# Kernel tuning notes

Measured on AMD Instinct MI355X. Metric: run time of the kernel, lower is better.

The kernel has to match this reference:

```python
import jax, jax.numpy as jnp
import numpy as np

B, T, C = 2, 2048, 1024
H, DH = 16, 64            # n_head, head_size; H*DH == C
HID = 4096                # FFN hidden
EPS = 1e-5


def setup_inputs() -> dict:
    key = jax.random.key(0)
    ks = jax.random.split(key, 16)
    s_c = 1.0 / np.sqrt(C)
    s_h = 1.0 / np.sqrt(HID)
    return {
        "x": jax.random.normal(ks[0], (B, T, C), jnp.float32),
        "ln1_g": jnp.ones((C,), jnp.float32),
        "ln1_b": jnp.zeros((C,), jnp.float32),
        "Wq": jax.random.normal(ks[1], (H, C, DH), jnp.float32) * s_c,
        "Wk": jax.random.normal(ks[2], (H, C, DH), jnp.float32) * s_c,
        "Wv": jax.random.normal(ks[3], (H, C, DH), jnp.float32) * s_c,
        "Wo": jax.random.normal(ks[4], (C, C), jnp.float32) * s_c,
        "bo": jnp.zeros((C,), jnp.float32),
        "ln2_g": jnp.ones((C,), jnp.float32),
        "ln2_b": jnp.zeros((C,), jnp.float32),
        "W1": jax.random.normal(ks[5], (C, HID), jnp.float32) * s_c,
        "b1": jnp.zeros((HID,), jnp.float32),
        "W2": jax.random.normal(ks[6], (HID, C), jnp.float32) * s_h,
        "b2": jnp.zeros((C,), jnp.float32),
    }


def _layernorm(x, g, b):
    mu = jnp.mean(x, axis=-1, keepdims=True)
    var = jnp.mean(jnp.square(x - mu), axis=-1, keepdims=True)
    return (x - mu) * jax.lax.rsqrt(var + EPS) * g + b


def _block(x, ln1_g, ln1_b, Wq, Wk, Wv, Wo, bo, ln2_g, ln2_b, W1, b1, W2, b2):
    # --- self-attention (note: scale by C**-0.5, as in original code) ---
    h = _layernorm(x, ln1_g, ln1_b)                      # [B,T,C]
    q = jnp.einsum("btc,hcd->bhtd", h, Wq)
    k = jnp.einsum("btc,hcd->bhtd", h, Wk)
    v = jnp.einsum("btc,hcd->bhtd", h, Wv)
    wei = jnp.einsum("bhtd,bhsd->bhts", q, k) * (C ** -0.5)
    causal = jnp.tril(jnp.ones((T, T), bool))            # [T,T]
    wei = jnp.where(causal, wei, -jnp.inf)
    wei = jax.nn.softmax(wei, axis=-1)
    att = jnp.einsum("bhts,bhsd->bhtd", wei, v)          # [B,H,T,DH]
    att = att.transpose(0, 2, 1, 3).reshape(x.shape[0], x.shape[1], C)  # concat heads
    x = x + att @ Wo + bo
    # --- feed-forward ---
    h2 = _layernorm(x, ln2_g, ln2_b)
    x = x + jax.nn.relu(h2 @ W1 + b1) @ W2 + b2
    return x


def reference(x, ln1_g, ln1_b, Wq, Wk, Wv, Wo, bo, ln2_g, ln2_b, W1, b1, W2, b2):
    return _block(x, ln1_g, ln1_b, Wq, Wk, Wv, Wo, bo, ln2_g, ln2_b, W1, b1, W2, b2)
```

## Files before the change

### kernel.cpp

```cpp
#include <hip/hip_runtime.h>

typedef unsigned short ushort_t;
typedef __attribute__((ext_vector_type(8))) short short8;
typedef __attribute__((ext_vector_type(4))) float f32x4;

#define BT 4096
#define TSEQ 2048
#define CC 1024
#define NH 16
#define DH 64
#define HID 4096
#define ATT_SCALE 0.03125f

__device__ __forceinline__ ushort_t f2bf(float f) {
    unsigned u = __float_as_uint(f);
    u = u + 0x7fffu + ((u >> 16) & 1u);
    return (ushort_t)(u >> 16);
}

typedef const __attribute__((address_space(1))) unsigned int* gptr_t;
typedef __attribute__((address_space(3))) unsigned int* lptr_t;
__device__ __forceinline__ void gload_lds16(const void* g, void* l) {
    __builtin_amdgcn_global_load_lds((gptr_t)g, (lptr_t)l, 16, 0, 0);
}

__global__ __launch_bounds__(256) void transpose_cvt(
    const float* __restrict__ in, ushort_t* __restrict__ out, int R, int Cn)
{
    __shared__ float tile[32][33];
    size_t off = (size_t)blockIdx.z * R * Cn;
    int c0 = blockIdx.x * 32, r0 = blockIdx.y * 32;
    int tx = threadIdx.x & 31, ty = threadIdx.x >> 5;
#pragma unroll
    for (int q = 0; q < 4; ++q)
        tile[ty + 8 * q][tx] = in[off + (size_t)(r0 + ty + 8 * q) * Cn + c0 + tx];
    __syncthreads();
#pragma unroll
    for (int q = 0; q < 4; ++q)
        out[off + (size_t)(c0 + ty + 8 * q) * R + r0 + tx] = f2bf(tile[tx][ty + 8 * q]);
}

__global__ __launch_bounds__(256) void ln_kernel(
    const float* __restrict__ x, const float* __restrict__ g,
    const float* __restrict__ b, ushort_t* __restrict__ out)
{
    int row = blockIdx.x;
    const float4 xv = ((const float4*)(x + (size_t)row * CC))[threadIdx.x];
    float s = xv.x + xv.y + xv.z + xv.w;
    float s2 = xv.x * xv.x + xv.y * xv.y + xv.z * xv.z + xv.w * xv.w;
#pragma unroll
    for (int d = 1; d < 64; d <<= 1) {
        s += __shfl_xor(s, d);
        s2 += __shfl_xor(s2, d);
    }
    __shared__ float ps[4], ps2[4];
    int w = threadIdx.x >> 6, lane = threadIdx.x & 63;
    if (lane == 0) { ps[w] = s; ps2[w] = s2; }
    __syncthreads();
    s = ps[0] + ps[1] + ps[2] + ps[3];
    s2 = ps2[0] + ps2[1] + ps2[2] + ps2[3];
    float mu = s * (1.0f / CC);
    float var = s2 * (1.0f / CC) - mu * mu;
    float rs = rsqrtf(var + 1e-5f);
    int c = threadIdx.x * 4;
    const float4 gv = ((const float4*)g)[threadIdx.x];
    const float4 bv = ((const float4*)b)[threadIdx.x];
    ushort_t u0 = f2bf((xv.x - mu) * rs * gv.x + bv.x);
    ushort_t u1 = f2bf((xv.y - mu) * rs * gv.y + bv.y);
    ushort_t u2 = f2bf((xv.z - mu) * rs * gv.z + bv.z);
    ushort_t u3 = f2bf((xv.w - mu) * rs * gv.w + bv.w);
    unsigned lo = (unsigned)u0 | ((unsigned)u1 << 16);
    unsigned hi = (unsigned)u2 | ((unsigned)u3 << 16);
    ((uint2*)(out + (size_t)row * CC + c))[0] = make_uint2(lo, hi);
}

template <int BM, int BN, int WM, int WN, int MR, int NR, int MODE>
__global__ __launch_bounds__(256) void gemm_tile(
    const ushort_t* __restrict__ A, const ushort_t* __restrict__ Bt,
    int N, int K,
    const float* __restrict__ bias, const float* __restrict__ resid,
    void* __restrict__ out0, void* __restrict__ out1, void* __restrict__ out2)
{
    static_assert(WM * WN == 4 && WM * MR * 16 == BM && WN * NR * 16 == BN, "geom");
    __shared__ ushort_t As[BM * 32];
    __shared__ ushort_t Bs[BN * 32];

    const int t = threadIdx.x;
    const int w = t >> 6, lane = t & 63, g = lane >> 4, c = lane & 15;
    const int wr = w / WN, wc = w % WN;
    const int m0 = blockIdx.x * BM;
    const int n0 = blockIdx.y * BN;

    f32x4 acc[MR][NR];
#pragma unroll
    for (int mi = 0; mi < MR; ++mi)
#pragma unroll
        for (int ni = 0; ni < NR; ++ni) acc[mi][ni] = f32x4{0.f, 0.f, 0.f, 0.f};

    const ushort_t* Ard = As + (size_t)(wr * MR * 16 + c) * 32 + g * 8;
    const ushort_t* Brd = Bs + (size_t)(wc * NR * 16 + c) * 32 + g * 8;
    const int arow = t >> 2, acol = (t & 3) * 8;

    for (int k0 = 0; k0 < K; k0 += 32) {
        __syncthreads();
#pragma unroll
        for (int j = 0; j < BM / 64; ++j)
            gload_lds16(A + (size_t)(m0 + j * 64 + arow) * K + k0 + acol,
                        As + (size_t)j * 2048 + t * 8);
#pragma unroll
        for (int j = 0; j < BN / 64; ++j)
            gload_lds16(Bt + (size_t)(n0 + j * 64 + arow) * K + k0 + acol,
                        Bs + (size_t)j * 2048 + t * 8);
        __syncthreads();

        short8 af[MR], bf[NR];
#pragma unroll
        for (int mi = 0; mi < MR; ++mi) af[mi] = *(const short8*)(Ard + mi * 512);
#pragma unroll
        for (int ni = 0; ni < NR; ++ni) bf[ni] = *(const short8*)(Brd + ni * 512);
#pragma unroll
        for (int mi = 0; mi < MR; ++mi)
#pragma unroll
            for (int ni = 0; ni < NR; ++ni)
                acc[mi][ni] = __builtin_amdgcn_mfma_f32_16x16x32_bf16(
                    af[mi], bf[ni], acc[mi][ni], 0, 0, 0);
    }

#pragma unroll
    for (int mi = 0; mi < MR; ++mi)
#pragma unroll
        for (int ni = 0; ni < NR; ++ni)
#pragma unroll
            for (int i = 0; i < 4; ++i) {
                int row = m0 + wr * MR * 16 + mi * 16 + g * 4 + i;
                int col = n0 + wc * NR * 16 + ni * 16 + c;
                float v = acc[mi][ni][i];
                if (MODE == 0) {
                    v += bias[col] + resid[(size_t)row * N + col];
                    ((float*)out0)[(size_t)row * N + col] = v;
                } else if (MODE == 1) {
                    v += bias[col];
                    v = v > 0.f ? v : 0.f;
                    ((ushort_t*)out0)[(size_t)row * N + col] = f2bf(v);
                } else {
                    int bb = row >> 11, tt = row & (TSEQ - 1);
                    if (col < 1024) {
                        int head = col >> 6, d = col & 63;
                        ((ushort_t*)out0)[((size_t)(bb * NH + head) * TSEQ + tt) * DH + d] =
                            f2bf(v * ATT_SCALE);
                    } else if (col < 2048) {
                        int head = (col - 1024) >> 6, d = col & 63;
                        ((ushort_t*)out1)[((size_t)(bb * NH + head) * TSEQ + tt) * DH + d] = f2bf(v);
                    } else {
                        int head = (col - 2048) >> 6, d = col & 63;
                        ((ushort_t*)out2)[((size_t)(bb * NH + head) * DH + d) * TSEQ + tt] = f2bf(v);
                    }
                }
            }
}

#define FLASH_BODY(st, kc, kn, PREF_COND, MASK_COND)                               \
    {                                                                              \
        const int S0 = (st) * 64;                                                  \
        short8 vv[4][2];                                                           \
        _Pragma("unroll") for (int nf = 0; nf < 4; ++nf)                           \
            _Pragma("unroll") for (int ks = 0; ks < 2; ++ks)                       \
                vv[nf][ks] = *(const short8*)(vp + (size_t)(nf * 16 + c) * TSEQ +  \
                                              S0 + ks * 32 + g * 8);               \
        if (PREF_COND) {                                                           \
            _Pragma("unroll") for (int sub = 0; sub < 4; ++sub)                    \
                _Pragma("unroll") for (int ks = 0; ks < 2; ++ks)                   \
                    kn[sub][ks] = *(const short8*)(kp +                            \
                        (size_t)(S0 + 64 + 16 * sub + c) * DH + ks * 32 + g * 8);  \
        }                                                                          \
        f32x4 sa[4];                                                               \
        _Pragma("unroll") for (int sub = 0; sub < 4; ++sub) {                      \
            f32x4 t0 = f32x4{0.f, 0.f, 0.f, 0.f};                                  \
            t0 = __builtin_amdgcn_mfma_f32_16x16x32_bf16(kc[sub][0], bq0, t0, 0, 0, 0); \
            t0 = __builtin_amdgcn_mfma_f32_16x16x32_bf16(kc[sub][1], bq1, t0, 0, 0, 0); \
            sa[sub] = t0;                                                          \
        }                                                                          \
        float pvv[16];                                                             \
        _Pragma("unroll") for (int sub = 0; sub < 4; ++sub)                        \
            _Pragma("unroll") for (int i = 0; i < 4; ++i) pvv[4 * sub + i] = sa[sub][i]; \
        if (MASK_COND) {                                                           \
            _Pragma("unroll") for (int sub = 0; sub < 4; ++sub)                    \
                _Pragma("unroll") for (int i = 0; i < 4; ++i)                      \
                    if (S0 + 16 * sub + 4 * g + i > q0 + c) pvv[4 * sub + i] = -INFINITY; \
        }                                                                          \
        float tmax = pvv[0];                                                       \
        _Pragma("unroll") for (int j = 1; j < 16; ++j) tmax = fmaxf(tmax, pvv[j]); \
        tmax = fmaxf(tmax, __shfl_xor(tmax, 16));                                  \
        tmax = fmaxf(tmax, __shfl_xor(tmax, 32));                                  \
        if (!__all(tmax - m_ <= 8.0f)) {                                           \
            float mn = fmaxf(m_, tmax);                                            \
            float fac = __expf(m_ - mn);                                           \
            m_ = mn;                                                               \
            l_ *= fac;                                                             \
            _Pragma("unroll") for (int i = 0; i < 4; ++i) {                        \
                float fr = __shfl(fac, 4 * g + i);                                 \
                _Pragma("unroll") for (int nf = 0; nf < 4; ++nf) o[nf][i] *= fr;   \
            }                                                                      \
        }                                                                          \
        float pp[16], rs = 0.f;                                                    \
        _Pragma("unroll") for (int j = 0; j < 16; ++j) {                           \
            pp[j] = __expf(pvv[j] - m_); rs += pp[j];                              \
        }                                                                          \
        rs += __shfl_xor(rs, 16);                                                  \
        rs += __shfl_xor(rs, 32);                                                  \
        l_ += rs;                                                                  \
        _Pragma("unroll") for (int sub = 0; sub < 4; ++sub) {                      \
            unsigned lo = (__float_as_uint(pp[4 * sub + 0]) >> 16) |               \
                          (__float_as_uint(pp[4 * sub + 1]) & 0xffff0000u);        \
            unsigned hi = (__float_as_uint(pp[4 * sub + 2]) >> 16) |               \
                          (__float_as_uint(pp[4 * sub + 3]) & 0xffff0000u);        \
            *(uint2*)(pw + 16 * sub + 4 * g) = make_uint2(lo, hi);                 \
        }                                                                          \
        asm volatile("s_waitcnt lgkmcnt(0)" ::: "memory");                         \
        short8 pa0 = *(const short8*)(&Plds[w][c * 72 + g * 8]);                   \
        short8 pa1 = *(const short8*)(&Plds[w][c * 72 + 32 + g * 8]);              \
        _Pragma("unroll") for (int nf = 0; nf < 4; ++nf) {                         \
            o[nf] = __builtin_amdgcn_mfma_f32_16x16x32_bf16(pa0, vv[nf][0], o[nf], 0, 0, 0); \
            o[nf] = __builtin_amdgcn_mfma_f32_16x16x32_bf16(pa1, vv[nf][1], o[nf], 0, 0, 0); \
        }                                                                          \
    }

__global__ __launch_bounds__(256) void flash_attn(
    const ushort_t* __restrict__ Q, const ushort_t* __restrict__ Kb,
    const ushort_t* __restrict__ Vt, ushort_t* __restrict__ attout)
{
    __shared__ ushort_t Plds[4][16 * 72];
    const int w = threadIdx.x >> 6, lane = threadIdx.x & 63;
    const int g = lane >> 4, c = lane & 15;
    const int bh = blockIdx.x, bb = bh >> 4, hh = bh & 15;
    const int q0 = blockIdx.y * 64 + w * 16;
    const ushort_t* qp = Q + (size_t)bh * TSEQ * DH;
    const ushort_t* kp = Kb + (size_t)bh * TSEQ * DH;
    const ushort_t* vp = Vt + (size_t)bh * DH * TSEQ;

    const short8 bq0 = *(const short8*)(qp + (size_t)(q0 + c) * DH + g * 8);
    const short8 bq1 = *(const short8*)(qp + (size_t)(q0 + c) * DH + 32 + g * 8);

    float m_ = -INFINITY, l_ = 0.f;
    f32x4 o[4];
#pragma unroll
    for (int nf = 0; nf < 4; ++nf) o[nf] = f32x4{0.f, 0.f, 0.f, 0.f};

    const int nst = q0 / 64 + 1;
    ushort_t* pw = &Plds[w][c * 72];

    short8 kkA[4][2], kkB[4][2];
#pragma unroll
    for (int sub = 0; sub < 4; ++sub)
#pragma unroll
        for (int ks = 0; ks < 2; ++ks)
            kkA[sub][ks] = *(const short8*)(kp + (size_t)(16 * sub + c) * DH + ks * 32 + g * 8);

    for (int st = 0; st < nst; st += 2) {
        FLASH_BODY(st, kkA, kkB, (st + 1 < nst), (st == nst - 1));
        if (st + 1 < nst) {
            const int st1 = st + 1;
            FLASH_BODY(st1, kkB, kkA, (st1 + 1 < nst), (st1 == nst - 1));
        }
    }

#pragma unroll
    for (int i = 0; i < 4; ++i) {
        float rl = 1.0f / __shfl(l_, 4 * g + i);
        int tt = q0 + 4 * g + i;
#pragma unroll
        for (int nf = 0; nf < 4; ++nf)
            attout[((size_t)(bb * TSEQ + tt)) * CC + hh * DH + nf * 16 + c] =
                f2bf(o[nf][i] * rl);
    }
}

__global__ __launch_bounds__(256) void flash_split(
    const ushort_t* __restrict__ Q, const ushort_t* __restrict__ Kb,
    const ushort_t* __restrict__ Vt, float* __restrict__ opart,
    float* __restrict__ mlpart, ushort_t* __restrict__ attout)
{
    __shared__ ushort_t Ks[64 * 64];
    __shared__ ushort_t Vs[64 * 64];
    __shared__ ushort_t Plds[4][16 * 72];
    const int t = threadIdx.x;
    const int w = t >> 6, lane = t & 63;
    const int g = lane >> 4, c = lane & 15;
    const int bh = blockIdx.x, qb = blockIdx.y, sc = blockIdx.z;
    if (sc * 8 > qb) return;
    const int bb = bh >> 4, hh = bh & 15;
    const int q0 = qb * 64 + w * 16;
    const ushort_t* qp = Q + (size_t)bh * TSEQ * DH;
    const char* kpB = (const char*)(Kb + (size_t)bh * TSEQ * DH);
    const char* vpB = (const char*)(Vt + (size_t)bh * DH * TSEQ);

    const short8 bq0 = *(const short8*)(qp + (size_t)(q0 + c) * DH + g * 8);
    const short8 bq1 = *(const short8*)(qp + (size_t)(q0 + c) * DH + 32 + g * 8);

    float m_ = -INFINITY, l_ = 0.f;
    f32x4 o[4];
#pragma unroll
    for (int nf = 0; nf < 4; ++nf) o[nf] = f32x4{0.f, 0.f, 0.f, 0.f};

    const int st0 = sc * 8;
    const int send = (st0 + 7 < qb) ? st0 + 7 : qb;
    ushort_t* pw = &Plds[w][c * 72];
    const unsigned bxor = (unsigned)((c & 7) << 4);

    const int srow = t >> 3, sb = (t & 7) * 16;
#define STAGE_KV(ST)                                                                \
    {                                                                               \
        const int S0_ = (ST) * 64;                                                  \
        _Pragma("unroll") for (int j = 0; j < 2; ++j) {                             \
            int r = j * 32 + srow;                                                  \
            int bs = sb ^ ((r & 7) << 4);                                           \
            gload_lds16(kpB + (size_t)(S0_ + r) * 128 + bs,                         \
                        (char*)Ks + r * 128 + sb);                                  \
            gload_lds16(vpB + (size_t)r * (TSEQ * 2) + S0_ * 2 + bs,                \
                        (char*)Vs + r * 128 + sb);                                  \
        }                                                                           \
    }

    STAGE_KV(st0);
    for (int st = st0; st <= send; ++st) {
        const int S0 = st * 64;
        __syncthreads();

        __builtin_amdgcn_s_setprio(1);
        f32x4 sa[4];
#pragma unroll
        for (int sub = 0; sub < 4; ++sub) {
            const char* kr = (const char*)Ks + (16 * sub + c) * 128;
            short8 k0 = *(const short8*)(kr + ((g * 16) ^ bxor));
            short8 k1 = *(const short8*)(kr + ((64 + g * 16) ^ bxor));
            f32x4 t0 = f32x4{0.f, 0.f, 0.f, 0.f};
            t0 = __builtin_amdgcn_mfma_f32_16x16x32_bf16(k0, bq0, t0, 0, 0, 0);
            t0 = __builtin_amdgcn_mfma_f32_16x16x32_bf16(k1, bq1, t0, 0, 0, 0);
            sa[sub] = t0;
        }
        __builtin_amdgcn_s_setprio(0);

        float pvv[16];
#pragma unroll
        for (int sub = 0; sub < 4; ++sub)
#pragma unroll
            for (int i = 0; i < 4; ++i) pvv[4 * sub + i] = sa[sub][i];
        if (st == qb) {
#pragma unroll
            for (int sub = 0; sub < 4; ++sub)
#pragma unroll
                for (int i = 0; i < 4; ++i)
                    if (S0 + 16 * sub + 4 * g + i > q0 + c) pvv[4 * sub + i] = -INFINITY;
        }
        float tmax = pvv[0];
#pragma unroll
        for (int j = 1; j < 16; ++j) tmax = fmaxf(tmax, pvv[j]);
        tmax = fmaxf(tmax, __shfl_xor(tmax, 16));
        tmax = fmaxf(tmax, __shfl_xor(tmax, 32));
        if (!__all(tmax - m_ <= 8.0f)) {
            float mn = fmaxf(m_, tmax);
            float fac = __expf(m_ - mn);
            m_ = mn;
            l_ *= fac;
#pragma unroll
            for (int i = 0; i < 4; ++i) {
                float fr = __shfl(fac, 4 * g + i);
#pragma unroll
                for (int nf = 0; nf < 4; ++nf) o[nf][i] *= fr;
            }
        }
        float pp[16], rs = 0.f;
#pragma unroll
        for (int j = 0; j < 16; ++j) { pp[j] = __expf(pvv[j] - m_); rs += pp[j]; }
        rs += __shfl_xor(rs, 16);
        rs += __shfl_xor(rs, 32);
        l_ += rs;

#pragma unroll
        for (int sub = 0; sub < 4; ++sub) {
            unsigned lo = (__float_as_uint(pp[4 * sub + 0]) >> 16) |
                          (__float_as_uint(pp[4 * sub + 1]) & 0xffff0000u);
            unsigned hi = (__float_as_uint(pp[4 * sub + 2]) >> 16) |
                          (__float_as_uint(pp[4 * sub + 3]) & 0xffff0000u);
            *(uint2*)(pw + 16 * sub + 4 * g) = make_uint2(lo, hi);
        }
        asm volatile("s_waitcnt lgkmcnt(0)" ::: "memory");
        short8 pa0 = *(const short8*)(&Plds[w][c * 72 + g * 8]);
        short8 pa1 = *(const short8*)(&Plds[w][c * 72 + 32 + g * 8]);

        __builtin_amdgcn_s_setprio(1);
#pragma unroll
        for (int nf = 0; nf < 4; ++nf) {
            const char* vr = (const char*)Vs + (nf * 16 + c) * 128;
            short8 v0 = *(const short8*)(vr + ((g * 16) ^ bxor));
            short8 v1 = *(const short8*)(vr + ((64 + g * 16) ^ bxor));
            o[nf] = __builtin_amdgcn_mfma_f32_16x16x32_bf16(pa0, v0, o[nf], 0, 0, 0);
            o[nf] = __builtin_amdgcn_mfma_f32_16x16x32_bf16(pa1, v1, o[nf], 0, 0, 0);
        }
        __builtin_amdgcn_s_setprio(0);

        __syncthreads();
        if (st < send) STAGE_KV(st + 1);
    }
#undef STAGE_KV

    if (qb < 8) {
#pragma unroll
        for (int i = 0; i < 4; ++i) {
            float rl = 1.0f / __shfl(l_, 4 * g + i);
            int tt = q0 + 4 * g + i;
#pragma unroll
            for (int nf = 0; nf < 4; ++nf)
                attout[((size_t)(bb * TSEQ + tt)) * CC + hh * DH + nf * 16 + c] =
                    f2bf(o[nf][i] * rl);
        }
    } else {
        const size_t slot = (size_t)(bh * 32 + qb) * 4 + sc;
        float* op = opart + slot * 4096;
#pragma unroll
        for (int nf = 0; nf < 4; ++nf)
#pragma unroll
            for (int i = 0; i < 4; ++i)
                op[(size_t)(w * 16 + 4 * g + i) * 64 + nf * 16 + c] = o[nf][i];
        if (g == 0) {
            mlpart[slot * 128 + w * 16 + c] = m_;
            mlpart[slot * 128 + 64 + w * 16 + c] = l_;
        }
    }
}

__global__ __launch_bounds__(256) void flash_combine(
    const float* __restrict__ opart, const float* __restrict__ mlpart,
    ushort_t* __restrict__ attout)
{
    const int bh = blockIdx.x, qb = blockIdx.y + 8;
    const int bb = bh >> 4, hh = bh & 15;
    const int nsc = (qb >> 3) + 1;
    const int t = threadIdx.x, r = t >> 2, qc = t & 3;
    const size_t slot0 = (size_t)(bh * 32 + qb) * 4;

    float mi[4], li[4];
    float M = -INFINITY;
#pragma unroll
    for (int i = 0; i < 4; ++i) {
        if (i < nsc) {
            mi[i] = mlpart[(slot0 + i) * 128 + r];
            li[i] = mlpart[(slot0 + i) * 128 + 64 + r];
            M = fmaxf(M, mi[i]);
        }
    }
    float L = 0.f;
    f32x4 acc[4];
#pragma unroll
    for (int j = 0; j < 4; ++j) acc[j] = f32x4{0.f, 0.f, 0.f, 0.f};
#pragma unroll
    for (int i = 0; i < 4; ++i) {
        if (i < nsc) {
            float F = __expf(mi[i] - M);
            L += li[i] * F;
            const f32x4* orow = (const f32x4*)(opart + (slot0 + i) * 4096 +
                                               (size_t)r * 64 + qc * 16);
#pragma unroll
            for (int j = 0; j < 4; ++j) acc[j] += orow[j] * F;
        }
    }
    float rl = 1.0f / L;
    unsigned wb[8];
#pragma unroll
    for (int j = 0; j < 4; ++j) {
        wb[2 * j] = (unsigned)f2bf(acc[j][0] * rl) | ((unsigned)f2bf(acc[j][1] * rl) << 16);
        wb[2 * j + 1] = (unsigned)f2bf(acc[j][2] * rl) | ((unsigned)f2bf(acc[j][3] * rl) << 16);
    }
    ushort_t* dst = attout + ((size_t)(bb * TSEQ + qb * 64 + r)) * CC + hh * DH + qc * 16;
    ((uint4*)dst)[0] = make_uint4(wb[0], wb[1], wb[2], wb[3]);
    ((uint4*)dst)[1] = make_uint4(wb[4], wb[5], wb[6], wb[7]);
}

extern "C" void kernel_launch(void* const* d_in, const int* in_sizes, int n_in,
                              void* d_out, int out_size, void* d_ws, size_t ws_size,
                              hipStream_t stream)
{
    (void)in_sizes; (void)n_in; (void)out_size;
    const float* x     = (const float*)d_in[0];
    const float* ln1_g = (const float*)d_in[1];
    const float* ln1_b = (const float*)d_in[2];
    const float* Wq    = (const float*)d_in[3];
    const float* Wk    = (const float*)d_in[4];
    const float* Wv    = (const float*)d_in[5];
    const float* Wo    = (const float*)d_in[6];
    const float* bo    = (const float*)d_in[7];
    const float* ln2_g = (const float*)d_in[8];
    const float* ln2_b = (const float*)d_in[9];
    const float* W1    = (const float*)d_in[10];
    const float* b1    = (const float*)d_in[11];
    const float* W2    = (const float*)d_in[12];
    const float* b2    = (const float*)d_in[13];

    char* p = (char*)d_ws;
    ushort_t* hbuf  = (ushort_t*)p;  p += (size_t)BT * CC * 2;
    ushort_t* WqkvT = (ushort_t*)p;  p += (size_t)3 * CC * CC * 2;
    ushort_t* WoT   = (ushort_t*)p;  p += (size_t)CC * CC * 2;
    ushort_t* W1T   = (ushort_t*)p;  p += (size_t)CC * HID * 2;
    ushort_t* W2T   = (ushort_t*)p;  p += (size_t)HID * CC * 2;
    ushort_t* Qb    = (ushort_t*)p;  p += (size_t)BT * CC * 2;
    ushort_t* Kbuf  = (ushort_t*)p;  p += (size_t)BT * CC * 2;
    ushort_t* Vt    = (ushort_t*)p;  p += (size_t)BT * CC * 2;
    ushort_t* atto  = (ushort_t*)p;  p += (size_t)BT * CC * 2;
    float*    x1    = (float*)p;     p += (size_t)BT * CC * 4;
    ushort_t* h2    = (ushort_t*)p;  p += (size_t)BT * CC * 2;
    ushort_t* mid   = (ushort_t*)p;  p += (size_t)BT * HID * 2;
    float*    opart = (float*)p;     p += (size_t)4096 * 4096 * 4;
    float*    mlprt = (float*)p;     p += (size_t)4096 * 128 * 4;
    const size_t need = (size_t)(p - (char*)d_ws);

    ushort_t* WqT = WqkvT;
    ushort_t* WkT = WqkvT + (size_t)CC * CC;
    ushort_t* WvT = WqkvT + (size_t)2 * CC * CC;

    dim3 blk(256);
    transpose_cvt<<<dim3(DH / 32, CC / 32, NH), blk, 0, stream>>>(Wq, WqT, CC, DH);
    transpose_cvt<<<dim3(DH / 32, CC / 32, NH), blk, 0, stream>>>(Wk, WkT, CC, DH);
    transpose_cvt<<<dim3(DH / 32, CC / 32, NH), blk, 0, stream>>>(Wv, WvT, CC, DH);
    transpose_cvt<<<dim3(CC / 32, CC / 32, 1), blk, 0, stream>>>(Wo, WoT, CC, CC);
    transpose_cvt<<<dim3(HID / 32, CC / 32, 1), blk, 0, stream>>>(W1, W1T, CC, HID);
    transpose_cvt<<<dim3(CC / 32, HID / 32, 1), blk, 0, stream>>>(W2, W2T, HID, CC);

    ln_kernel<<<dim3(BT), blk, 0, stream>>>(x, ln1_g, ln1_b, hbuf);
    gemm_tile<128, 128, 2, 2, 4, 4, 2><<<dim3(BT / 128, 3072 / 128), blk, 0, stream>>>(
        hbuf, WqkvT, 3072, CC, nullptr, nullptr, Qb, Kbuf, Vt);
    if (ws_size >= need) {
        flash_split<<<dim3(2 * NH, TSEQ / 64, 4), blk, 0, stream>>>(
            Qb, Kbuf, Vt, opart, mlprt, atto);
        flash_combine<<<dim3(2 * NH, TSEQ / 64 - 8), blk, 0, stream>>>(opart, mlprt, atto);
    } else {
        flash_attn<<<dim3(2 * NH, TSEQ / 64), blk, 0, stream>>>(Qb, Kbuf, Vt, atto);
    }
    gemm_tile<128, 64, 4, 1, 2, 4, 0><<<dim3(BT / 128, CC / 64), blk, 0, stream>>>(
        atto, WoT, CC, CC, bo, x, (void*)x1, nullptr, nullptr);
    ln_kernel<<<dim3(BT), blk, 0, stream>>>(x1, ln2_g, ln2_b, h2);
    gemm_tile<128, 128, 2, 2, 4, 4, 1><<<dim3(BT / 128, HID / 128), blk, 0, stream>>>(
        h2, W1T, HID, CC, b1, nullptr, (void*)mid, nullptr, nullptr);
    gemm_tile<128, 64, 4, 1, 2, 4, 0><<<dim3(BT / 128, CC / 64), blk, 0, stream>>>(
        mid, W2T, CC, HID, b2, x1, d_out, nullptr, nullptr);
}
```

Before: 281.4 us.

## Split FFN2 GEMM along K into four partials with separate combine kernel

Adds a split-K mode to the tiled GEMM so the second FFN projection runs as four K-slices over a 3D grid, writing fp32 partials into the existing attention workspace. A new elementwise kernel sums the partials and adds bias and residual. This raises block count and shortens each block's K loop to improve CU utilization, at the cost of extra global memory traffic for partials and one more launch. Leading-dimension parameters are added to the GEMM to support slicing.

```diff
diff --git a/kernel.cpp b/kernel.cpp
--- a/kernel.cpp
+++ b/kernel.cpp
@@ -77,7 +77,7 @@
 template <int BM, int BN, int WM, int WN, int MR, int NR, int MODE>
 __global__ __launch_bounds__(256) void gemm_tile(
     const ushort_t* __restrict__ A, const ushort_t* __restrict__ Bt,
-    int N, int K,
+    int N, int K, int lda, int ldb,
     const float* __restrict__ bias, const float* __restrict__ resid,
     void* __restrict__ out0, void* __restrict__ out1, void* __restrict__ out2)
 {
@@ -90,6 +90,10 @@
     const int wr = w / WN, wc = w % WN;
     const int m0 = blockIdx.x * BM;
     const int n0 = blockIdx.y * BN;
+    if (MODE == 3) {
+        A += (size_t)blockIdx.z * K;
+        Bt += (size_t)blockIdx.z * K;
+    }
 
     f32x4 acc[MR][NR];
 #pragma unroll
@@ -105,11 +109,11 @@
         __syncthreads();
 #pragma unroll
         for (int j = 0; j < BM / 64; ++j)
-            gload_lds16(A + (size_t)(m0 + j * 64 + arow) * K + k0 + acol,
+            gload_lds16(A + (size_t)(m0 + j * 64 + arow) * lda + k0 + acol,
                         As + (size_t)j * 2048 + t * 8);
 #pragma unroll
         for (int j = 0; j < BN / 64; ++j)
-            gload_lds16(Bt + (size_t)(n0 + j * 64 + arow) * K + k0 + acol,
+            gload_lds16(Bt + (size_t)(n0 + j * 64 + arow) * ldb + k0 + acol,
                         Bs + (size_t)j * 2048 + t * 8);
         __syncthreads();
 
@@ -142,6 +146,8 @@
                     v += bias[col];
                     v = v > 0.f ? v : 0.f;
                     ((ushort_t*)out0)[(size_t)row * N + col] = f2bf(v);
+                } else if (MODE == 3) {
+                    ((float*)out0)[(size_t)blockIdx.z * BT * N + (size_t)row * N + col] = v;
                 } else {
                     int bb = row >> 11, tt = row & (TSEQ - 1);
                     if (col < 1024) {
@@ -157,6 +163,28 @@
                     }
                 }
             }
+}
+
+__global__ __launch_bounds__(256) void ffn2_combine(
+    const float* __restrict__ parts, const float* __restrict__ bias,
+    const float* __restrict__ resid, float* __restrict__ out)
+{
+    const size_t idx = (size_t)blockIdx.x * 256 + threadIdx.x;
+    const size_t off = idx * 4;
+    const size_t m = off >> 10, col = off & 1023;
+    float4 a0 = ((const float4*)(parts + (size_t)0 * BT * CC + off))[0];
+    float4 a1 = ((const float4*)(parts + (size_t)1 * BT * CC + off))[0];
+    float4 a2 = ((const float4*)(parts + (size_t)2 * BT * CC + off))[0];
+    float4 a3 = ((const float4*)(parts + (size_t)3 * BT * CC + off))[0];
+    float4 bv = ((const float4*)(bias + col))[0];
+    float4 rv = ((const float4*)(resid + off))[0];
+    float4 o;
+    o.x = a0.x + a1.x + a2.x + a3.x + bv.x + rv.x;
+    o.y = a0.y + a1.y + a2.y + a3.y + bv.y + rv.y;
+    o.z = a0.z + a1.z + a2.z + a3.z + bv.z + rv.z;
+    o.w = a0.w + a1.w + a2.w + a3.w + bv.w + rv.w;
+    ((float4*)(out + off))[0] = o;
+    (void)m;
 }
 
 #define FLASH_BODY(st, kc, kn, PREF_COND, MASK_COND)                               \
@@ -527,7 +555,7 @@
 
     ln_kernel<<<dim3(BT), blk, 0, stream>>>(x, ln1_g, ln1_b, hbuf);
     gemm_tile<128, 128, 2, 2, 4, 4, 2><<<dim3(BT / 128, 3072 / 128), blk, 0, stream>>>(
-        hbuf, WqkvT, 3072, CC, nullptr, nullptr, Qb, Kbuf, Vt);
+        hbuf, WqkvT, 3072, CC, CC, CC, nullptr, nullptr, Qb, Kbuf, Vt);
     if (ws_size >= need) {
         flash_split<<<dim3(2 * NH, TSEQ / 64, 4), blk, 0, stream>>>(
             Qb, Kbuf, Vt, opart, mlprt, atto);
@@ -536,10 +564,16 @@
         flash_attn<<<dim3(2 * NH, TSEQ / 64), blk, 0, stream>>>(Qb, Kbuf, Vt, atto);
     }
     gemm_tile<128, 64, 4, 1, 2, 4, 0><<<dim3(BT / 128, CC / 64), blk, 0, stream>>>(
-        atto, WoT, CC, CC, bo, x, (void*)x1, nullptr, nullptr);
+        atto, WoT, CC, CC, CC, CC, bo, x, (void*)x1, nullptr, nullptr);
     ln_kernel<<<dim3(BT), blk, 0, stream>>>(x1, ln2_g, ln2_b, h2);
     gemm_tile<128, 128, 2, 2, 4, 4, 1><<<dim3(BT / 128, HID / 128), blk, 0, stream>>>(
-        h2, W1T, HID, CC, b1, nullptr, (void*)mid, nullptr, nullptr);
-    gemm_tile<128, 64, 4, 1, 2, 4, 0><<<dim3(BT / 128, CC / 64), blk, 0, stream>>>(
-        mid, W2T, CC, HID, b2, x1, d_out, nullptr, nullptr);
-}
+        h2, W1T, HID, CC, CC, CC, b1, nullptr, (void*)mid, nullptr, nullptr);
+    if (ws_size >= need) {
+        gemm_tile<128, 64, 4, 1, 2, 4, 3><<<dim3(BT / 128, CC / 64, 4), blk, 0, stream>>>(
+            mid, W2T, CC, HID / 4, HID, HID, nullptr, nullptr, (void*)opart, nullptr, nullptr);
+        ffn2_combine<<<dim3(BT * CC / 4 / 256), blk, 0, stream>>>(opart, b2, x1, (float*)d_out);
+    } else {
+        gemm_tile<128, 64, 4, 1, 2, 4, 0><<<dim3(BT / 128, CC / 64), blk, 0, stream>>>(
+            mid, W2T, CC, HID, HID, HID, b2, x1, d_out, nullptr, nullptr);
+    }
+}
```

Result: no change. 284.7 us (+1.2%).

## Double-buffer GEMM LDS loads and split-K the FFN down-projection

Applied to the files above, without the earlier changes.

The GEMM main loop now uses two LDS buffers: the next K-slice is issued asynchronously while the current one is computed, with explicit vmcnt waits and raised wave priority around the MFMA block. The W2 GEMM is split along K into two halves running in parallel over blockIdx.z. Each half writes a bf16 partial, and a new combine kernel adds the partials, bias and residual. The unused fallback flash_attn path is removed. This overlaps global loads with compute and doubles the parallelism of the FFN2 GEMM. In exchange it costs more LDS, an extra partial-sum round trip through memory, and bf16 rounding of the partials.

```diff
diff --git a/kernel.cpp b/kernel.cpp
--- a/kernel.cpp
+++ b/kernel.cpp
@@ -16,6 +16,9 @@
     unsigned u = __float_as_uint(f);
     u = u + 0x7fffu + ((u >> 16) & 1u);
     return (ushort_t)(u >> 16);
+}
+__device__ __forceinline__ float bf2f(ushort_t u) {
+    return __uint_as_float(((unsigned)u) << 16);
 }
 
 typedef const __attribute__((address_space(1))) unsigned int* gptr_t;
@@ -77,19 +80,23 @@
 template <int BM, int BN, int WM, int WN, int MR, int NR, int MODE>
 __global__ __launch_bounds__(256) void gemm_tile(
     const ushort_t* __restrict__ A, const ushort_t* __restrict__ Bt,
-    int N, int K,
+    int N, int K, int lda, int ldb,
     const float* __restrict__ bias, const float* __restrict__ resid,
     void* __restrict__ out0, void* __restrict__ out1, void* __restrict__ out2)
 {
     static_assert(WM * WN == 4 && WM * MR * 16 == BM && WN * NR * 16 == BN, "geom");
-    __shared__ ushort_t As[BM * 32];
-    __shared__ ushort_t Bs[BN * 32];
+    __shared__ ushort_t As[2][BM * 32];
+    __shared__ ushort_t Bs[2][BN * 32];
 
     const int t = threadIdx.x;
     const int w = t >> 6, lane = t & 63, g = lane >> 4, c = lane & 15;
     const int wr = w / WN, wc = w % WN;
     const int m0 = blockIdx.x * BM;
     const int n0 = blockIdx.y * BN;
+    if (MODE == 3) {
+        A += (size_t)blockIdx.z * K;
+        Bt += (size_t)blockIdx.z * K;
+    }
 
     f32x4 acc[MR][NR];
 #pragma unroll
@@ -97,34 +104,56 @@
 #pragma unroll
         for (int ni = 0; ni < NR; ++ni) acc[mi][ni] = f32x4{0.f, 0.f, 0.f, 0.f};
 
-    const ushort_t* Ard = As + (size_t)(wr * MR * 16 + c) * 32 + g * 8;
-    const ushort_t* Brd = Bs + (size_t)(wc * NR * 16 + c) * 32 + g * 8;
     const int arow = t >> 2, acol = (t & 3) * 8;
-
+    const int aoff = (wr * MR * 16 + c) * 32 + g * 8;
+    const int boff = (wc * NR * 16 + c) * 32 + g * 8;
+
+#define STAGE(BUF, K0)                                                          \
+    {                                                                           \
+        _Pragma("unroll") for (int j = 0; j < BM / 64; ++j)                     \
+            gload_lds16(A + (size_t)(m0 + j * 64 + arow) * lda + (K0) + acol,   \
+                        As[BUF] + (size_t)j * 2048 + t * 8);                    \
+        _Pragma("unroll") for (int j = 0; j < BN / 64; ++j)                     \
+            gload_lds16(Bt + (size_t)(n0 + j * 64 + arow) * ldb + (K0) + acol,  \
+                        Bs[BUF] + (size_t)j * 2048 + t * 8);                    \
+    }
+
+    STAGE(0, 0);
+    int cur = 0;
     for (int k0 = 0; k0 < K; k0 += 32) {
-        __syncthreads();
-#pragma unroll
-        for (int j = 0; j < BM / 64; ++j)
-            gload_lds16(A + (size_t)(m0 + j * 64 + arow) * K + k0 + acol,
-                        As + (size_t)j * 2048 + t * 8);
-#pragma unroll
-        for (int j = 0; j < BN / 64; ++j)
-            gload_lds16(Bt + (size_t)(n0 + j * 64 + arow) * K + k0 + acol,
-                        Bs + (size_t)j * 2048 + t * 8);
-        __syncthreads();
-
+        if (k0 + 32 < K) {
+            STAGE(cur ^ 1, k0 + 32);
+            if constexpr (BM / 64 + BN / 64 == 4)
+                asm volatile("s_waitcnt vmcnt(4)" ::: "memory");
+            else
+                asm volatile("s_waitcnt vmcnt(3)" ::: "memory");
+        } else {
+            asm volatile("s_waitcnt vmcnt(0)" ::: "memory");
+        }
+        __builtin_amdgcn_sched_barrier(0);
+        __builtin_amdgcn_s_barrier();
+
+        const ushort_t* Ard = As[cur] + aoff;
+        const ushort_t* Brd = Bs[cur] + boff;
         short8 af[MR], bf[NR];
 #pragma unroll
         for (int mi = 0; mi < MR; ++mi) af[mi] = *(const short8*)(Ard + mi * 512);
 #pragma unroll
         for (int ni = 0; ni < NR; ++ni) bf[ni] = *(const short8*)(Brd + ni * 512);
+        __builtin_amdgcn_s_setprio(1);
 #pragma unroll
         for (int mi = 0; mi < MR; ++mi)
 #pragma unroll
             for (int ni = 0; ni < NR; ++ni)
                 acc[mi][ni] = __builtin_amdgcn_mfma_f32_16x16x32_bf16(
                     af[mi], bf[ni], acc[mi][ni], 0, 0, 0);
-    }
+        __builtin_amdgcn_s_setprio(0);
+
+        __builtin_amdgcn_sched_barrier(0);
+        __builtin_amdgcn_s_barrier();
+        cur ^= 1;
+    }
+#undef STAGE
 
 #pragma unroll
     for (int mi = 0; mi < MR; ++mi)
@@ -142,6 +171,9 @@
                     v += bias[col];
                     v = v > 0.f ? v : 0.f;
                     ((ushort_t*)out0)[(size_t)row * N + col] = f2bf(v);
+                } else if (MODE == 3) {
+                    ((ushort_t*)out0)[(size_t)blockIdx.z * BT * N + (size_t)row * N + col] =
+                        f2bf(v);
                 } else {
                     int bb = row >> 11, tt = row & (TSEQ - 1);
                     if (col < 1024) {
@@ -159,120 +191,28 @@
             }
 }
 
-#define FLASH_BODY(st, kc, kn, PREF_COND, MASK_COND)                               \
-    {                                                                              \
-        const int S0 = (st) * 64;                                                  \
-        short8 vv[4][2];                                                           \
-        _Pragma("unroll") for (int nf = 0; nf < 4; ++nf)                           \
-            _Pragma("unroll") for (int ks = 0; ks < 2; ++ks)                       \
-                vv[nf][ks] = *(const short8*)(vp + (size_t)(nf * 16 + c) * TSEQ +  \
-                                              S0 + ks * 32 + g * 8);               \
-        if (PREF_COND) {                                                           \
-            _Pragma("unroll") for (int sub = 0; sub < 4; ++sub)                    \
-                _Pragma("unroll") for (int ks = 0; ks < 2; ++ks)                   \
-                    kn[sub][ks] = *(const short8*)(kp +                            \
-                        (size_t)(S0 + 64 + 16 * sub + c) * DH + ks * 32 + g * 8);  \
-        }                                                                          \
-        f32x4 sa[4];                                                               \
-        _Pragma("unroll") for (int sub = 0; sub < 4; ++sub) {                      \
-            f32x4 t0 = f32x4{0.f, 0.f, 0.f, 0.f};                                  \
-            t0 = __builtin_amdgcn_mfma_f32_16x16x32_bf16(kc[sub][0], bq0, t0, 0, 0, 0); \
-            t0 = __builtin_amdgcn_mfma_f32_16x16x32_bf16(kc[sub][1], bq1, t0, 0, 0, 0); \
-            sa[sub] = t0;                                                          \
-        }                                                                          \
-        float pvv[16];                                                             \
-        _Pragma("unroll") for (int sub = 0; sub < 4; ++sub)                        \
-            _Pragma("unroll") for (int i = 0; i < 4; ++i) pvv[4 * sub + i] = sa[sub][i]; \
-        if (MASK_COND) {                                                           \
-            _Pragma("unroll") for (int sub = 0; sub < 4; ++sub)                    \
-                _Pragma("unroll") for (int i = 0; i < 4; ++i)                      \
-                    if (S0 + 16 * sub + 4 * g + i > q0 + c) pvv[4 * sub + i] = -INFINITY; \
-        }                                                                          \
-        float tmax = pvv[0];                                                       \
-        _Pragma("unroll") for (int j = 1; j < 16; ++j) tmax = fmaxf(tmax, pvv[j]); \
-        tmax = fmaxf(tmax, __shfl_xor(tmax, 16));                                  \
-        tmax = fmaxf(tmax, __shfl_xor(tmax, 32));                                  \
-        if (!__all(tmax - m_ <= 8.0f)) {                                           \
-            float mn = fmaxf(m_, tmax);                                            \
-            float fac = __expf(m_ - mn);                                           \
-            m_ = mn;                                                               \
-            l_ *= fac;                                                             \
-            _Pragma("unroll") for (int i = 0; i < 4; ++i) {                        \
-                float fr = __shfl(fac, 4 * g + i);                                 \
-                _Pragma("unroll") for (int nf = 0; nf < 4; ++nf) o[nf][i] *= fr;   \
-            }                                                                      \
-        }                                                                          \
-        float pp[16], rs = 0.f;                                                    \
-        _Pragma("unroll") for (int j = 0; j < 16; ++j) {                           \
-            pp[j] = __expf(pvv[j] - m_); rs += pp[j];                              \
-        }                                                                          \
-        rs += __shfl_xor(rs, 16);                                                  \
-        rs += __shfl_xor(rs, 32);                                                  \
-        l_ += rs;                                                                  \
-        _Pragma("unroll") for (int sub = 0; sub < 4; ++sub) {                      \
-            unsigned lo = (__float_as_uint(pp[4 * sub + 0]) >> 16) |               \
-                          (__float_as_uint(pp[4 * sub + 1]) & 0xffff0000u);        \
-            unsigned hi = (__float_as_uint(pp[4 * sub + 2]) >> 16) |               \
-                          (__float_as_uint(pp[4 * sub + 3]) & 0xffff0000u);        \
-            *(uint2*)(pw + 16 * sub + 4 * g) = make_uint2(lo, hi);                 \
-        }                                                                          \
-        asm volatile("s_waitcnt lgkmcnt(0)" ::: "memory");                         \
-        short8 pa0 = *(const short8*)(&Plds[w][c * 72 + g * 8]);                   \
-        short8 pa1 = *(const short8*)(&Plds[w][c * 72 + 32 + g * 8]);              \
-        _Pragma("unroll") for (int nf = 0; nf < 4; ++nf) {                         \
-            o[nf] = __builtin_amdgcn_mfma_f32_16x16x32_bf16(pa0, vv[nf][0], o[nf], 0, 0, 0); \
-            o[nf] = __builtin_amdgcn_mfma_f32_16x16x32_bf16(pa1, vv[nf][1], o[nf], 0, 0, 0); \
-        }                                                                          \
-    }
-
-__global__ __launch_bounds__(256) void flash_attn(
-    const ushort_t* __restrict__ Q, const ushort_t* __restrict__ Kb,
-    const ushort_t* __restrict__ Vt, ushort_t* __restrict__ attout)
-{
-    __shared__ ushort_t Plds[4][16 * 72];
-    const int w = threadIdx.x >> 6, lane = threadIdx.x & 63;
-    const int g = lane >> 4, c = lane & 15;
-    const int bh = blockIdx.x, bb = bh >> 4, hh = bh & 15;
-    const int q0 = blockIdx.y * 64 + w * 16;
-    const ushort_t* qp = Q + (size_t)bh * TSEQ * DH;
-    const ushort_t* kp = Kb + (size_t)bh * TSEQ * DH;
-    const ushort_t* vp = Vt + (size_t)bh * DH * TSEQ;
-
-    const short8 bq0 = *(const short8*)(qp + (size_t)(q0 + c) * DH + g * 8);
-    const short8 bq1 = *(const short8*)(qp + (size_t)(q0 + c) * DH + 32 + g * 8);
-
-    float m_ = -INFINITY, l_ = 0.f;
-    f32x4 o[4];
-#pragma unroll
-    for (int nf = 0; nf < 4; ++nf) o[nf] = f32x4{0.f, 0.f, 0.f, 0.f};
-
-    const int nst = q0 / 64 + 1;
-    ushort_t* pw = &Plds[w][c * 72];
-
-    short8 kkA[4][2], kkB[4][2];
-#pragma unroll
-    for (int sub = 0; sub < 4; ++sub)
-#pragma unroll
-        for (int ks = 0; ks < 2; ++ks)
-            kkA[sub][ks] = *(const short8*)(kp + (size_t)(16 * sub + c) * DH + ks * 32 + g * 8);
-
-    for (int st = 0; st < nst; st += 2) {
-        FLASH_BODY(st, kkA, kkB, (st + 1 < nst), (st == nst - 1));
-        if (st + 1 < nst) {
-            const int st1 = st + 1;
-            FLASH_BODY(st1, kkB, kkA, (st1 + 1 < nst), (st1 == nst - 1));
-        }
-    }
-
-#pragma unroll
-    for (int i = 0; i < 4; ++i) {
-        float rl = 1.0f / __shfl(l_, 4 * g + i);
-        int tt = q0 + 4 * g + i;
-#pragma unroll
-        for (int nf = 0; nf < 4; ++nf)
-            attout[((size_t)(bb * TSEQ + tt)) * CC + hh * DH + nf * 16 + c] =
-                f2bf(o[nf][i] * rl);
-    }
+__global__ __launch_bounds__(256) void ffn2_combine(
+    const ushort_t* __restrict__ parts, const float* __restrict__ bias,
+    const float* __restrict__ resid, float* __restrict__ out)
+{
+    const size_t off = ((size_t)blockIdx.x * 256 + threadIdx.x) * 8;
+    const int col = (int)(off & 1023);
+    short8 p0 = *(const short8*)(parts + off);
+    short8 p1 = *(const short8*)(parts + (size_t)BT * CC + off);
+    float4 r0 = ((const float4*)(resid + off))[0];
+    float4 r1 = ((const float4*)(resid + off + 4))[0];
+    float4 b0 = ((const float4*)(bias + col))[0];
+    float4 b1 = ((const float4*)(bias + col + 4))[0];
+    float o[8];
+#pragma unroll
+    for (int j = 0; j < 8; ++j)
+        o[j] = bf2f((ushort_t)p0[j]) + bf2f((ushort_t)p1[j]);
+    float4 w0 = make_float4(o[0] + b0.x + r0.x, o[1] + b0.y + r0.y,
+                            o[2] + b0.z + r0.z, o[3] + b0.w + r0.w);
+    float4 w1 = make_float4(o[4] + b1.x + r1.x, o[5] + b1.y + r1.y,
+                            o[6] + b1.z + r1.z, o[7] + b1.w + r1.w);
+    ((float4*)(out + off))[0] = w0;
+    ((float4*)(out + off + 4))[0] = w1;
 }
 
 __global__ __launch_bounds__(256) void flash_split(
@@ -480,7 +420,7 @@
                               void* d_out, int out_size, void* d_ws, size_t ws_size,
                               hipStream_t stream)
 {
-    (void)in_sizes; (void)n_in; (void)out_size;
+    (void)in_sizes; (void)n_in; (void)out_size; (void)ws_size;
     const float* x     = (const float*)d_in[0];
     const float* ln1_g = (const float*)d_in[1];
     const float* ln1_b = (const float*)d_in[2];
@@ -511,7 +451,6 @@
     ushort_t* mid   = (ushort_t*)p;  p += (size_t)BT * HID * 2;
     float*    opart = (float*)p;     p += (size_t)4096 * 4096 * 4;
     float*    mlprt = (float*)p;     p += (size_t)4096 * 128 * 4;
-    const size_t need = (size_t)(p - (char*)d_ws);
 
     ushort_t* WqT = WqkvT;
     ushort_t* WkT = WqkvT + (size_t)CC * CC;
@@ -527,19 +466,17 @@
 
     ln_kernel<<<dim3(BT), blk, 0, stream>>>(x, ln1_g, ln1_b, hbuf);
     gemm_tile<128, 128, 2, 2, 4, 4, 2><<<dim3(BT / 128, 3072 / 128), blk, 0, stream>>>(
-        hbuf, WqkvT, 3072, CC, nullptr, nullptr, Qb, Kbuf, Vt);
-    if (ws_size >= need) {
-        flash_split<<<dim3(2 * NH, TSEQ / 64, 4), blk, 0, stream>>>(
-            Qb, Kbuf, Vt, opart, mlprt, atto);
-        flash_combine<<<dim3(2 * NH, TSEQ / 64 - 8), blk, 0, stream>>>(opart, mlprt, atto);
-    } else {
-        flash_attn<<<dim3(2 * NH, TSEQ / 64), blk, 0, stream>>>(Qb, Kbuf, Vt, atto);
-    }
+        hbuf, WqkvT, 3072, CC, CC, CC, nullptr, nullptr, Qb, Kbuf, Vt);
+    flash_split<<<dim3(2 * NH, TSEQ / 64, 4), blk, 0, stream>>>(
+        Qb, Kbuf, Vt, opart, mlprt, atto);
+    flash_combine<<<dim3(2 * NH, TSEQ / 64 - 8), blk, 0, stream>>>(opart, mlprt, atto);
     gemm_tile<128, 64, 4, 1, 2, 4, 0><<<dim3(BT / 128, CC / 64), blk, 0, stream>>>(
-        atto, WoT, CC, CC, bo, x, (void*)x1, nullptr, nullptr);
+        atto, WoT, CC, CC, CC, CC, bo, x, (void*)x1, nullptr, nullptr);
     ln_kernel<<<dim3(BT), blk, 0, stream>>>(x1, ln2_g, ln2_b, h2);
     gemm_tile<128, 128, 2, 2, 4, 4, 1><<<dim3(BT / 128, HID / 128), blk, 0, stream>>>(
-        h2, W1T, HID, CC, b1, nullptr, (void*)mid, nullptr, nullptr);
-    gemm_tile<128, 64, 4, 1, 2, 4, 0><<<dim3(BT / 128, CC / 64), blk, 0, stream>>>(
-        mid, W2T, CC, HID, b2, x1, d_out, nullptr, nullptr);
-}
+        h2, W1T, HID, CC, CC, CC, b1, nullptr, (void*)mid, nullptr, nullptr);
+    gemm_tile<128, 64, 4, 1, 2, 4, 3><<<dim3(BT / 128, CC / 64, 2), blk, 0, stream>>>(
+        mid, W2T, CC, HID / 2, HID, HID, nullptr, nullptr, (void*)opart, nullptr, nullptr);
+    ffn2_combine<<<dim3(BT * CC / 8 / 256), blk, 0, stream>>>(
+        (const ushort_t*)opart, b2, x1, (float*)d_out);
+}
```

Result: faster. 255.7 us (-9.1%).
